# Kernel optimization log

Hardware: AMD Instinct MI355X
Metric: run time of the kernel (lower is better)

Reference implementation:

```python
import jax, jax.numpy as jnp
import numpy as np

N_NODES = 100000
N_EDGES = 400000
N_GRAPHS = 2500
DIM = 128
F_IN = 78
N_LAYERS = 3
BN_EPS = 1e-5


def setup_inputs() -> dict:
    key = jax.random.key(0)
    ks = jax.random.split(key, 24)
    def lin(k, fi, fo):
        return jax.random.normal(k, (fi, fo), jnp.float32) / np.sqrt(fi)
    inp = {
        "x": jax.random.normal(ks[0], (N_NODES, F_IN), jnp.float32),
        "edge_index": jax.random.randint(ks[1], (2, N_EDGES), 0, N_NODES, jnp.int32),
        "batch": jnp.sort(jax.random.randint(ks[2], (N_NODES,), 0, N_GRAPHS, jnp.int32)),
        "num_graphs": N_GRAPHS,
        "gcn1_W": lin(ks[3], F_IN, DIM), "gcn1_b": jnp.zeros((DIM,), jnp.float32),
        "gcn2_W": lin(ks[4], DIM, DIM), "gcn2_b": jnp.zeros((DIM,), jnp.float32),
        "gin0_w1": lin(ks[5], F_IN, DIM), "gin0_b1": jnp.zeros((DIM,), jnp.float32),
        "gin0_w2": lin(ks[6], DIM, DIM), "gin0_b2": jnp.zeros((DIM,), jnp.float32),
        # layers 1..2 stacked (same 128->128 shapes)
        "gin_w1": jnp.stack([lin(ks[7], DIM, DIM), lin(ks[8], DIM, DIM)]),
        "gin_b1": jnp.zeros((2, DIM), jnp.float32),
        "gin_w2": jnp.stack([lin(ks[9], DIM, DIM), lin(ks[10], DIM, DIM)]),
        "gin_b2": jnp.zeros((2, DIM), jnp.float32),
        "bn_gamma": jnp.ones((N_LAYERS, DIM), jnp.float32),
        "bn_beta": jnp.zeros((N_LAYERS, DIM), jnp.float32),
    }
    return inp


def reference(x, edge_index, batch, num_graphs,
              gcn1_W, gcn1_b, gcn2_W, gcn2_b,
              gin0_w1, gin0_b1, gin0_w2, gin0_b2,
              gin_w1, gin_b1, gin_w2, gin_b2,
              bn_gamma, bn_beta):
    n = x.shape[0]
    src, dst = edge_index[0], edge_index[1]

    def gcn(h, W, b):
        # linear -> symmetric-normalized aggregation with self loops (PyG GCNConv)
        h = h @ W
        loop = jnp.arange(n, dtype=src.dtype)
        s = jnp.concatenate([src, loop])
        d = jnp.concatenate([dst, loop])
        deg = jax.ops.segment_sum(jnp.ones(s.shape[0], h.dtype), d, num_segments=n)
        dis = jax.lax.rsqrt(deg)  # deg >= 1 thanks to self loops
        norm = (dis[s] * dis[d])[:, None]
        return jax.ops.segment_sum(h[s] * norm, d, num_segments=n) + b

    def gin(h, w1, b1, w2, b2):
        # GINConv, eps=0: mlp(x + sum_{j->i} x_j)
        agg = jax.ops.segment_sum(h[src], dst, num_segments=n)
        z = jax.nn.relu((h + agg) @ w1 + b1)
        return z @ w2 + b2

    def bn(h, g, bt):
        mu = h.mean(0)
        var = ((h - mu) ** 2).mean(0)
        return (h - mu) * jax.lax.rsqrt(var + BN_EPS) * g + bt

    g1 = jax.nn.relu(gcn(x, gcn1_W, gcn1_b))
    g2 = jax.nn.relu(gcn(g1, gcn2_W, gcn2_b))
    g2a = g2 + g1
    g2m = g2 * g1

    h = x
    xs = []
    m = jnp.float32(1.0)
    e = jnp.float32(0.0)
    for i in range(N_LAYERS):
        if i == 0:
            h = gin(h, gin0_w1, gin0_b1, gin0_w2, gin0_b2)
        else:
            h = gin(h, gin_w1[i - 1], gin_b1[i - 1], gin_w2[i - 1], gin_b2[i - 1])
        h = bn(jax.nn.relu(h), bn_gamma[i], bn_beta[i])
        m = m * h
        e = e + h
        xs.append(h)

    rep = jnp.concatenate(xs + [m, e, g1, g2, g2a, g2m], axis=-1)  # [N, 9*DIM]
    return jax.ops.segment_max(rep, batch, num_segments=num_graphs)
```

## Files before the change

### kernel.cpp

```cpp
#include <hip/hip_runtime.h>
#include <math.h>

#define DIMC 128
#define FINC 78
#define REPW 1152
#define SCAN_TILE 1024

typedef __attribute__((ext_vector_type(8))) short short8x;
typedef __attribute__((ext_vector_type(4))) float f32x4;
typedef unsigned int u32;
typedef const __attribute__((address_space(1))) u32* gas_u32p;
typedef __attribute__((address_space(3))) u32* las_u32p;

__device__ inline float b2f(unsigned short u) {
    union { unsigned int i; float f; } v; v.i = ((unsigned int)u) << 16; return v.f;
}
__device__ inline unsigned short f2b(float f) {
    union { float f; unsigned int i; } v; v.f = f;
    unsigned int r = (v.i + 0x7FFFu + ((v.i >> 16) & 1u)) >> 16;
    return (unsigned short)r;
}

__device__ __forceinline__ void gld16(const void* g, void* l) {
    __builtin_amdgcn_global_load_lds((gas_u32p)g, (las_u32p)l, 16, 0, 0);
}


__global__ void k_fill_int(int* __restrict__ p, int v, int n) {
    int i = blockIdx.x * blockDim.x + threadIdx.x;
    if (i < n) p[i] = v;
}

__global__ void k_fill(float* __restrict__ p, float v, int n) {
    int i = blockIdx.x * blockDim.x + threadIdx.x;
    if (i < n) p[i] = v;
}

__global__ void k_count(const int* __restrict__ dst, int* __restrict__ cnt, int E) {
    int e = blockIdx.x * blockDim.x + threadIdx.x;
    if (e < E) atomicAdd(&cnt[dst[e]], 1);
}

__launch_bounds__(256)
__global__ void k_tilesum(const int* __restrict__ cnt, int* __restrict__ tileSum, int N) {
    __shared__ int red[256];
    int base = blockIdx.x * SCAN_TILE;
    int s = 0;
    for (int i = threadIdx.x; i < SCAN_TILE; i += 256) {
        int idx = base + i;
        if (idx < N) s += cnt[idx];
    }
    red[threadIdx.x] = s;
    __syncthreads();
    for (int d = 128; d > 0; d >>= 1) {
        if (threadIdx.x < d) red[threadIdx.x] += red[threadIdx.x + d];
        __syncthreads();
    }
    if (threadIdx.x == 0) tileSum[blockIdx.x] = red[0];
}

__launch_bounds__(256)
__global__ void k_tilescan(const int* __restrict__ tileSum, int* __restrict__ tileOff,
                           int* __restrict__ rowptr, int T, int N) {
    __shared__ int sh[256];
    int t = threadIdx.x;
    int orig = (t < T) ? tileSum[t] : 0;
    sh[t] = orig;
    __syncthreads();
    for (int d = 1; d < 256; d <<= 1) {
        int v = (t >= d) ? sh[t - d] : 0;
        __syncthreads();
        sh[t] += v;
        __syncthreads();
    }
    if (t < T) tileOff[t] = sh[t] - orig;
    if (t == 255) rowptr[N] = sh[255];
}

__launch_bounds__(256)
__global__ void k_tileemit(const int* __restrict__ cnt, const int* __restrict__ tileOff,
                           int* __restrict__ rowptr, int* __restrict__ cursor,
                           float* __restrict__ dis, int N) {
    __shared__ int sh[256];
    int t = threadIdx.x;
    int base = blockIdx.x * SCAN_TILE;
    int idx0 = base + t * 4;
    int v0 = 0, v1 = 0, v2 = 0, v3 = 0;
    if (idx0 + 3 < N) {
        int4 v = *(const int4*)(cnt + idx0);
        v0 = v.x; v1 = v.y; v2 = v.z; v3 = v.w;
    } else {
        if (idx0 + 0 < N) v0 = cnt[idx0 + 0];
        if (idx0 + 1 < N) v1 = cnt[idx0 + 1];
        if (idx0 + 2 < N) v2 = cnt[idx0 + 2];
        if (idx0 + 3 < N) v3 = cnt[idx0 + 3];
    }
    int s0 = v0, s1 = s0 + v1, s2 = s1 + v2, s3 = s2 + v3;
    sh[t] = s3;
    __syncthreads();
    for (int d = 1; d < 256; d <<= 1) {
        int v = (t >= d) ? sh[t - d] : 0;
        __syncthreads();
        sh[t] += v;
        __syncthreads();
    }
    int gbase = tileOff[blockIdx.x] + ((t == 0) ? 0 : sh[t - 1]);
    int ex[4] = {0, s0, s1, s2};
    int vv[4] = {v0, v1, v2, v3};
#pragma unroll
    for (int j = 0; j < 4; ++j) {
        int idx = idx0 + j;
        if (idx < N) {
            int r = gbase + ex[j];
            rowptr[idx] = r;
            cursor[idx] = r;
            dis[idx] = rsqrtf((float)vv[j] + 1.0f);
        }
    }
}

__global__ void k_scatter(const int* __restrict__ src, const int* __restrict__ dst,
                          int* __restrict__ cursor, int* __restrict__ col, int E) {
    int e = blockIdx.x * blockDim.x + threadIdx.x;
    if (e < E) {
        int pos = atomicAdd(&cursor[dst[e]], 1);
        col[pos] = src[e];
    }
}

__global__ void k_bounds(const int* __restrict__ batch, int* __restrict__ start, int N, int G) {
    int g = blockIdx.x * blockDim.x + threadIdx.x;
    if (g <= G) {
        int lo = 0, hi = N;
        while (lo < hi) { int mid = (lo + hi) >> 1; if (batch[mid] < g) lo = mid + 1; else hi = mid; }
        start[g] = lo;
    }
}


__global__ void k_cvt_w(const float* __restrict__ s0, const float* __restrict__ s1,
                        const float* __restrict__ s2, const float* __restrict__ s3,
                        const float* __restrict__ s4, const float* __restrict__ s5,
                        const float* __restrict__ s6, const float* __restrict__ s7,
                        unsigned short* __restrict__ whi, unsigned short* __restrict__ wlo) {
    int my = blockIdx.y;
    const float* src; int Ksrc, KP; size_t dstoff;
    const size_t o96 = (size_t)128 * 96, o128 = (size_t)128 * 128;
    switch (my) {
        case 0: src = s0; Ksrc = 78;  KP = 96;  dstoff = 0; break;
        case 1: src = s1; Ksrc = 78;  KP = 96;  dstoff = o96; break;
        case 2: src = s2; Ksrc = 128; KP = 128; dstoff = 2 * o96; break;
        case 3: src = s3; Ksrc = 128; KP = 128; dstoff = 2 * o96 + o128; break;
        case 4: src = s4; Ksrc = 128; KP = 128; dstoff = 2 * o96 + 2 * o128; break;
        case 5: src = s5; Ksrc = 128; KP = 128; dstoff = 2 * o96 + 3 * o128; break;
        case 6: src = s6; Ksrc = 128; KP = 128; dstoff = 2 * o96 + 4 * o128; break;
        default: src = s7; Ksrc = 128; KP = 128; dstoff = 2 * o96 + 5 * o128; break;
    }
    int i = blockIdx.x * blockDim.x + threadIdx.x;
    if (i < 128 * KP) {
        int n = i / KP, k = i - n * KP;
        float v = (k < Ksrc) ? src[(size_t)k * DIMC + n] : 0.f;
        unsigned short hi = f2b(v);
        unsigned short lo = f2b(v - b2f(hi));
        whi[dstoff + i] = hi;
        wlo[dstoff + i] = lo;
    }
}


__global__ void k_pack_x(const float* __restrict__ x, unsigned short* __restrict__ xhi,
                         unsigned short* __restrict__ xlo, int N) {
    int i = blockIdx.x * blockDim.x + threadIdx.x;
    int r = i / 24, cc = (i - r * 24) * 4;
    if (r >= N) return;
    float v[4];
#pragma unroll
    for (int j = 0; j < 4; ++j) { int k = cc + j; v[j] = (k < FINC) ? x[(size_t)r * FINC + k] : 0.f; }
    unsigned short h[4], l[4];
#pragma unroll
    for (int j = 0; j < 4; ++j) { h[j] = f2b(v[j]); l[j] = f2b(v[j] - b2f(h[j])); }
    *(ushort4*)(xhi + (size_t)r * 96 + cc) = make_ushort4(h[0], h[1], h[2], h[3]);
    *(ushort4*)(xlo + (size_t)r * 96 + cc) = make_ushort4(l[0], l[1], l[2], l[3]);
}


template<int KP, bool SPLITA, bool STATS>
__launch_bounds__(256, 3)
__global__ void k_gemm_f(const void* __restrict__ A0, const void* __restrict__ A1,
                         const unsigned short* __restrict__ Bhi, const unsigned short* __restrict__ Blo,
                         const float* __restrict__ bias, const float* __restrict__ rowScale,
                         float* __restrict__ statsOut, float* __restrict__ C,
                         int N, int doRelu) {
    constexpr int NT = KP / 32;
    __shared__ unsigned short lds[2][2][4096];
    __shared__ float sStats[256];
    const int tid = threadIdx.x;
    const int wave = tid >> 6, lane = tid & 63;
    const int lm = lane & 15, q = lane >> 4;
    const int row = blockIdx.x * 64 + wave * 16 + lm;
    const int am = (row < N) ? row : (N - 1);

    const int rr = tid & 127;
    const int g0 = tid >> 7;
    const int o0 = ((g0 ^ (rr & 3)) << 3);
    const int o1 = (((2 + g0) ^ (rr & 3)) << 3);
    const size_t brow = (size_t)rr * KP;
    const int u0 = tid << 3;
    const int u1 = (256 + tid) << 3;

    auto stageB = [&](int c, int d) {
        const int cb = c << 5;
        gld16(Bhi + brow + cb + o0, &lds[d][0][u0]);
        gld16(Bhi + brow + cb + o1, &lds[d][0][u1]);
        gld16(Blo + brow + cb + o0, &lds[d][1][u0]);
        gld16(Blo + brow + cb + o1, &lds[d][1][u1]);
    };

    const unsigned short* aph = nullptr;
    const unsigned short* apl = nullptr;
    const float* apf = nullptr;
    if constexpr (SPLITA) {
        aph = (const unsigned short*)A0 + (size_t)am * KP;
        apl = (const unsigned short*)A1 + (size_t)am * KP;
    } else {
        apf = (const float*)A0 + (size_t)am * KP;
    }

    short8x pah, pal, nah, nal;
    float4 pf0, pf1, nf0, nf1;

    auto loadA = [&](int c, short8x& h, short8x& l, float4& f0, float4& f1) {
        int ko = c * 32 + q * 8;
        if constexpr (SPLITA) {
            h = *(const short8x*)(aph + ko);
            l = *(const short8x*)(apl + ko);
        } else {
            f0 = *(const float4*)(apf + ko);
            f1 = *(const float4*)(apf + ko + 4);
        }
    };

    f32x4 acc[8];
#pragma unroll
    for (int i = 0; i < 8; ++i) acc[i] = (f32x4){0.f, 0.f, 0.f, 0.f};

    stageB(0, 0);
    loadA(0, pah, pal, pf0, pf1);
    __builtin_amdgcn_sched_barrier(0);

#pragma unroll
    for (int t = 0; t < NT; ++t) {
        const int cur = t & 1;
        if (t + 1 < NT) {
            stageB(t + 1, cur ^ 1);
            loadA(t + 1, nah, nal, nf0, nf1);
            __builtin_amdgcn_sched_barrier(0);
            asm volatile("s_waitcnt vmcnt(6)" ::: "memory");
        } else {
            asm volatile("s_waitcnt vmcnt(0)" ::: "memory");
        }
        __builtin_amdgcn_s_barrier();
        __builtin_amdgcn_sched_barrier(0);

        short8x ah, al;
        if constexpr (SPLITA) {
            ah = pah; al = pal;
        } else {
            float f[8] = {pf0.x, pf0.y, pf0.z, pf0.w, pf1.x, pf1.y, pf1.z, pf1.w};
#pragma unroll
            for (int j = 0; j < 8; ++j) {
                unsigned short h = f2b(f[j]);
                ah[j] = (short)h;
                al[j] = (short)f2b(f[j] - b2f(h));
            }
        }
#pragma unroll
        for (int ct = 0; ct < 8; ++ct) {
            int n = ct * 16 + lm;
            int sl = ((q ^ (n & 3)) * 128 + n) << 3;
            short8x bh = *(const short8x*)&lds[cur][0][sl];
            short8x bl = *(const short8x*)&lds[cur][1][sl];
            acc[ct] = __builtin_amdgcn_mfma_f32_16x16x32_bf16(bh, ah, acc[ct], 0, 0, 0);
            acc[ct] = __builtin_amdgcn_mfma_f32_16x16x32_bf16(bh, al, acc[ct], 0, 0, 0);
            acc[ct] = __builtin_amdgcn_mfma_f32_16x16x32_bf16(bl, ah, acc[ct], 0, 0, 0);
        }
        __builtin_amdgcn_s_barrier();
        pah = nah; pal = nal; pf0 = nf0; pf1 = nf1;
    }

    if constexpr (STATS) { sStats[tid] = 0.f; __syncthreads(); }
    const bool valid = row < N;
    float sc = 1.f;
    if (rowScale) sc = rowScale[valid ? row : 0];

#pragma unroll
    for (int ct = 0; ct < 8; ++ct) {
        float vv[4];
#pragma unroll
        for (int i = 0; i < 4; ++i) {
            float v = acc[ct][i];
            if (bias) v += bias[ct * 16 + q * 4 + i];
            if (doRelu) v = fmaxf(v, 0.f);
            v *= sc;
            vv[i] = valid ? v : 0.f;
        }
        if (valid)
            *(float4*)(C + (size_t)row * DIMC + ct * 16 + q * 4) =
                make_float4(vv[0], vv[1], vv[2], vv[3]);
        if constexpr (STATS) {
#pragma unroll
            for (int i = 0; i < 4; ++i) {
                float vs = vv[i], vq = vv[i] * vv[i];
#pragma unroll
                for (int o = 1; o < 16; o <<= 1) { vs += __shfl_xor(vs, o); vq += __shfl_xor(vq, o); }
                if (lm == 0) {
                    int colg = ct * 16 + q * 4 + i;
                    atomicAdd(&sStats[colg], vs);
                    atomicAdd(&sStats[DIMC + colg], vq);
                }
            }
        }
    }
    if constexpr (STATS) {
        __syncthreads();
        atomicAdd(&statsOut[tid], sStats[tid]);
    }
}


__global__ void k_bn_coef(const float* __restrict__ bnsum, const float* __restrict__ gamma,
                          const float* __restrict__ beta, float* __restrict__ coef, float invN) {
    int c = threadIdx.x;
    float mu  = bnsum[c] * invN;
    float var = bnsum[128 + c] * invN - mu * mu;
    float inv = rsqrtf(var + 1e-5f);
    float s = gamma[c] * inv;
    coef[c] = s;
    coef[128 + c] = beta[c] - mu * s;
}


__global__ void k_fold_w(const float* __restrict__ w1, const float* __restrict__ coefL,
                         unsigned short* __restrict__ fwhi, unsigned short* __restrict__ fwlo,
                         float* __restrict__ cvec) {
    __shared__ float red[128];
    int n = blockIdx.x, k = threadIdx.x;
    float w = w1[(size_t)k * DIMC + n];
    float ws = w * coefL[k];
    unsigned short h = f2b(ws);
    fwhi[(size_t)n * DIMC + k] = h;
    fwlo[(size_t)n * DIMC + k] = f2b(ws - b2f(h));
    red[k] = w * coefL[DIMC + k];
    __syncthreads();
    for (int d = 64; d > 0; d >>= 1) { if (k < d) red[k] += red[k + d]; __syncthreads(); }
    if (k == 0) cvec[n] = red[0];
}


__global__ void k_gather_gcn(const float4* __restrict__ t, const int* __restrict__ rowptr,
                             const int* __restrict__ col, const float* __restrict__ dis,
                             const float4* __restrict__ bias, float4* __restrict__ out, int N) {
    int i = blockIdx.x * blockDim.x + threadIdx.x;
    int node = i >> 5, c4 = i & 31;
    if (node >= N) return;
    int s = rowptr[node], e = rowptr[node + 1];
    float4 acc = t[(size_t)node * 32 + c4];
    for (int k = s; k < e; ++k) {
        float4 v = t[(size_t)col[k] * 32 + c4];
        acc.x += v.x; acc.y += v.y; acc.z += v.z; acc.w += v.w;
    }
    float d = dis[node];
    float4 b = bias[c4];
    float4 o;
    o.x = fmaxf(acc.x * d + b.x, 0.f);
    o.y = fmaxf(acc.y * d + b.y, 0.f);
    o.z = fmaxf(acc.z * d + b.z, 0.f);
    o.w = fmaxf(acc.w * d + b.w, 0.f);
    out[(size_t)node * 32 + c4] = o;
}

__global__ void k_gather_gin(const float4* __restrict__ t, const int* __restrict__ rowptr,
                             const int* __restrict__ col, const float4* __restrict__ bias,
                             float4* __restrict__ out, int N) {
    int i = blockIdx.x * blockDim.x + threadIdx.x;
    int node = i >> 5, c4 = i & 31;
    if (node >= N) return;
    int s = rowptr[node], e = rowptr[node + 1];
    float4 acc = t[(size_t)node * 32 + c4];
    for (int k = s; k < e; ++k) {
        float4 v = t[(size_t)col[k] * 32 + c4];
        acc.x += v.x; acc.y += v.y; acc.z += v.z; acc.w += v.w;
    }
    float4 b = bias[c4];
    float4 o;
    o.x = fmaxf(acc.x + b.x, 0.f);
    o.y = fmaxf(acc.y + b.y, 0.f);
    o.z = fmaxf(acc.z + b.z, 0.f);
    o.w = fmaxf(acc.w + b.w, 0.f);
    out[(size_t)node * 32 + c4] = o;
}


__global__ void k_segmax_gin_all(const float* __restrict__ h0, const float* __restrict__ h1,
                                 const float* __restrict__ h2, const float* __restrict__ coef,
                                 const int* __restrict__ start, float* __restrict__ out) {
    int g = blockIdx.x, c = threadIdx.x;
    float s0 = coef[c],       t0 = coef[128 + c];
    float s1 = coef[256 + c], t1 = coef[384 + c];
    float s2 = coef[512 + c], t2 = coef[640 + c];
    int s = start[g], e = start[g + 1];
    float m0 = -INFINITY, m1 = -INFINITY, m2 = -INFINITY, mm = -INFINITY, me = -INFINITY;
    for (int n = s; n < e; ++n) {
        size_t idx = (size_t)n * DIMC + c;
        float a0 = fmaf(h0[idx], s0, t0);
        float a1 = fmaf(h1[idx], s1, t1);
        float a2 = fmaf(h2[idx], s2, t2);
        m0 = fmaxf(m0, a0); m1 = fmaxf(m1, a1); m2 = fmaxf(m2, a2);
        mm = fmaxf(mm, a0 * a1 * a2);
        me = fmaxf(me, a0 + a1 + a2);
    }
    size_t o = (size_t)g * REPW + c;
    out[o]            = m0;
    out[o + 1 * DIMC] = m1;
    out[o + 2 * DIMC] = m2;
    out[o + 3 * DIMC] = mm;
    out[o + 4 * DIMC] = me;
}

__global__ void k_segmax_gcn(const float* __restrict__ G1, const float* __restrict__ G2,
                             const int* __restrict__ start, float* __restrict__ out) {
    int g = blockIdx.x, c = threadIdx.x;
    int s = start[g], e = start[g + 1];
    float m1 = -INFINITY, m2 = -INFINITY, ma = -INFINITY, mm = -INFINITY;
    for (int n = s; n < e; ++n) {
        float a = G1[(size_t)n * DIMC + c], b = G2[(size_t)n * DIMC + c];
        m1 = fmaxf(m1, a); m2 = fmaxf(m2, b);
        ma = fmaxf(ma, a + b); mm = fmaxf(mm, a * b);
    }
    size_t o = (size_t)g * REPW + c;
    out[o + 5 * DIMC] = m1;
    out[o + 6 * DIMC] = m2;
    out[o + 7 * DIMC] = ma;
    out[o + 8 * DIMC] = mm;
}


extern "C" void kernel_launch(void* const* d_in, const int* in_sizes, int n_in,
                              void* d_out, int out_size, void* d_ws, size_t ws_size,
                              hipStream_t stream) {
    const float* x       = (const float*)d_in[0];
    const int*   ei      = (const int*)d_in[1];
    const int*   batch   = (const int*)d_in[2];
    const float* gcn1_W  = (const float*)d_in[4];
    const float* gcn1_b  = (const float*)d_in[5];
    const float* gcn2_W  = (const float*)d_in[6];
    const float* gcn2_b  = (const float*)d_in[7];
    const float* gin0_w1 = (const float*)d_in[8];
    const float* gin0_b1 = (const float*)d_in[9];
    const float* gin0_w2 = (const float*)d_in[10];
    const float* gin0_b2 = (const float*)d_in[11];
    const float* gin_w1  = (const float*)d_in[12];
    const float* gin_b1  = (const float*)d_in[13];
    const float* gin_w2  = (const float*)d_in[14];
    const float* gin_b2  = (const float*)d_in[15];
    const float* bn_g    = (const float*)d_in[16];
    const float* bn_b    = (const float*)d_in[17];
    float* out = (float*)d_out;

    const int N = in_sizes[0] / FINC;
    const int E = in_sizes[1] / 2;
    const int G = out_size / REPW;
    const int* srcv = ei;
    const int* dstv = ei + E;

    char* ws = (char*)d_ws;
    size_t off = 0;
    auto alloc = [&](size_t bytes) { char* p = ws + off; off += (bytes + 255) & ~(size_t)255; return p; };
    int*   cnt     = (int*)alloc((size_t)N * 4);
    int*   rowptr  = (int*)alloc(((size_t)N + 1) * 4);
    int*   cursor  = (int*)alloc((size_t)N * 4);
    int*   col     = (int*)alloc((size_t)E * 4);
    float* dis     = (float*)alloc((size_t)N * 4);
    float* bnsum   = (float*)alloc(768 * 4);
    float* coef    = (float*)alloc(768 * 4);
    float* cvec    = (float*)alloc(128 * 4);
    int*   start   = (int*)alloc(((size_t)G + 1) * 4);
    int*   tileSum = (int*)alloc(256 * 4);
    int*   tileOff = (int*)alloc(256 * 4);
    const size_t o96 = (size_t)128 * 96, o128 = (size_t)128 * 128;
    const size_t wtElems = 2 * o96 + 6 * o128;
    unsigned short* whi  = (unsigned short*)alloc(wtElems * 2);
    unsigned short* wlo  = (unsigned short*)alloc(wtElems * 2);
    unsigned short* fwhi = (unsigned short*)alloc(o128 * 2);
    unsigned short* fwlo = (unsigned short*)alloc(o128 * 2);
    const size_t fbytes = (size_t)N * DIMC * 4;
    float* bufT = (float*)alloc(fbytes);
    float* bufZ = (float*)alloc(fbytes);
    float* h0   = (float*)alloc(fbytes);
    float* h1   = (float*)alloc(fbytes);
    float* h2   = (float*)alloc(fbytes);
    unsigned short* xhi = (unsigned short*)h1;
    unsigned short* xlo = (unsigned short*)h1 + (size_t)N * 96;
    (void)ws_size; (void)n_in;

    const size_t woff[8] = {0, o96, 2 * o96, 2 * o96 + o128, 2 * o96 + 2 * o128,
                            2 * o96 + 3 * o128, 2 * o96 + 4 * o128, 2 * o96 + 5 * o128};

    const int T = 256;
    auto cdiv = [](long a, long b) { return (int)((a + b - 1) / b); };
    const int gemmGrid = cdiv(N, 64);
    const int gatherGrid = cdiv((long)N * 32, T);
    const int nTiles = cdiv(N, SCAN_TILE);
    const float invN = 1.0f / (float)N;

    k_fill_int<<<cdiv(N, T), T, 0, stream>>>(cnt, 0, N);
    k_count<<<cdiv(E, T), T, 0, stream>>>(dstv, cnt, E);
    k_tilesum<<<nTiles, T, 0, stream>>>(cnt, tileSum, N);
    k_tilescan<<<1, T, 0, stream>>>(tileSum, tileOff, rowptr, nTiles, N);
    k_tileemit<<<nTiles, T, 0, stream>>>(cnt, tileOff, rowptr, cursor, dis, N);
    k_scatter<<<cdiv(E, T), T, 0, stream>>>(srcv, dstv, cursor, col, E);
    k_bounds<<<cdiv(G + 1, T), T, 0, stream>>>(batch, start, N, G);
    k_fill<<<3, T, 0, stream>>>(bnsum, 0.f, 768);
    {
        dim3 g(64, 8);
        k_cvt_w<<<g, T, 0, stream>>>(gcn1_W, gin0_w1, gcn2_W, gin0_w2,
                                     gin_w1, gin_w1 + o128, gin_w2, gin_w2 + o128, whi, wlo);
    }
    k_pack_x<<<cdiv((long)N * 24, T), T, 0, stream>>>(x, xhi, xlo, N);

    k_gemm_f<96, true, false><<<gemmGrid, T, 0, stream>>>(xhi, xlo, whi + woff[0], wlo + woff[0],
                                                          nullptr, dis, nullptr, bufT, N, 0);
    k_gather_gcn<<<gatherGrid, T, 0, stream>>>((const float4*)bufT, rowptr, col, dis,
                                               (const float4*)gcn1_b, (float4*)bufZ, N);
    k_gemm_f<128, false, false><<<gemmGrid, T, 0, stream>>>(bufZ, nullptr, whi + woff[2], wlo + woff[2],
                                                            nullptr, dis, nullptr, bufT, N, 0);
    k_gather_gcn<<<gatherGrid, T, 0, stream>>>((const float4*)bufT, rowptr, col, dis,
                                               (const float4*)gcn2_b, (float4*)h0, N);
    k_segmax_gcn<<<G, DIMC, 0, stream>>>(bufZ, h0, start, out);

    k_gemm_f<96, true, false><<<gemmGrid, T, 0, stream>>>(xhi, xlo, whi + woff[1], wlo + woff[1],
                                                          nullptr, nullptr, nullptr, bufT, N, 0);
    k_gather_gin<<<gatherGrid, T, 0, stream>>>((const float4*)bufT, rowptr, col,
                                               (const float4*)gin0_b1, (float4*)bufZ, N);
    k_gemm_f<128, false, true><<<gemmGrid, T, 0, stream>>>(bufZ, nullptr, whi + woff[3], wlo + woff[3],
                                                           gin0_b2, nullptr, bnsum, h0, N, 1);
    k_bn_coef<<<1, DIMC, 0, stream>>>(bnsum, bn_g, bn_b, coef, invN);
    k_fold_w<<<DIMC, DIMC, 0, stream>>>(gin_w1, coef, fwhi, fwlo, cvec);

    k_gemm_f<128, false, false><<<gemmGrid, T, 0, stream>>>(h0, nullptr, fwhi, fwlo,
                                                            cvec, nullptr, nullptr, bufT, N, 0);
    k_gather_gin<<<gatherGrid, T, 0, stream>>>((const float4*)bufT, rowptr, col,
                                               (const float4*)gin_b1, (float4*)bufZ, N);
    k_gemm_f<128, false, true><<<gemmGrid, T, 0, stream>>>(bufZ, nullptr, whi + woff[6], wlo + woff[6],
                                                           gin_b2, nullptr, bnsum + 256, h1, N, 1);
    k_bn_coef<<<1, DIMC, 0, stream>>>(bnsum + 256, bn_g + DIMC, bn_b + DIMC, coef + 256, invN);
    k_fold_w<<<DIMC, DIMC, 0, stream>>>(gin_w1 + o128, coef + 256, fwhi, fwlo, cvec);

    k_gemm_f<128, false, false><<<gemmGrid, T, 0, stream>>>(h1, nullptr, fwhi, fwlo,
                                                            cvec, nullptr, nullptr, bufT, N, 0);
    k_gather_gin<<<gatherGrid, T, 0, stream>>>((const float4*)bufT, rowptr, col,
                                               (const float4*)(gin_b1 + DIMC), (float4*)bufZ, N);
    k_gemm_f<128, false, true><<<gemmGrid, T, 0, stream>>>(bufZ, nullptr, whi + woff[7], wlo + woff[7],
                                                           gin_b2 + DIMC, nullptr, bnsum + 512, h2, N, 1);
    k_bn_coef<<<1, DIMC, 0, stream>>>(bnsum + 512, bn_g + 2 * DIMC, bn_b + 2 * DIMC, coef + 512, invN);

    k_segmax_gin_all<<<G, DIMC, 0, stream>>>(h0, h1, h2, coef, start, out);
}
```

Before: 818.0 us.

## Make GEMM persistent with full B resident in LDS and 32-row wave strips

Turns the split-bf16 GEMM into a persistent kernel with a fixed grid of 768 or 512 blocks. Each block loads the whole 128-wide weight matrix (hi and lo) into LDS once, then its waves loop over independent 32-row strips with no block barriers inside the loop. BN statistics now accumulate in registers across strips and are reduced only once per block, which cuts shared and global atomics. The cost is more LDS and registers per block (two accumulator sets, launch bounds lowered to 2), plus possible load imbalance from the fixed grid.

After: 1.125 ms. +37.5%, slower.

```diff
diff --git a/kernel.cpp b/kernel.cpp
--- a/kernel.cpp
+++ b/kernel.cpp
@@ -184,133 +184,174 @@
 }
 
 
+#define LOADA(c, H0, L0, H1, L1, F00, F01, F10, F11)                           \
+    {                                                                          \
+        const int ko_ = (c) * 32 + q * 8;                                      \
+        if constexpr (SPLITA) {                                                \
+            H0 = *(const short8x*)(aph0 + ko_);                                \
+            L0 = *(const short8x*)(apl0 + ko_);                                \
+            H1 = *(const short8x*)(aph1 + ko_);                                \
+            L1 = *(const short8x*)(apl1 + ko_);                                \
+        } else {                                                               \
+            F00 = *(const float4*)(apf0 + ko_);                                \
+            F01 = *(const float4*)(apf0 + ko_ + 4);                            \
+            F10 = *(const float4*)(apf1 + ko_);                                \
+            F11 = *(const float4*)(apf1 + ko_ + 4);                            \
+        }                                                                      \
+    }
+
+#define CVT8(F0, F1, H, L)                                                     \
+    {                                                                          \
+        float ff_[8] = {F0.x, F0.y, F0.z, F0.w, F1.x, F1.y, F1.z, F1.w};       \
+        _Pragma("unroll")                                                      \
+        for (int j_ = 0; j_ < 8; ++j_) {                                       \
+            unsigned short hh_ = f2b(ff_[j_]);                                 \
+            H[j_] = (short)hh_;                                                \
+            L[j_] = (short)f2b(ff_[j_] - b2f(hh_));                            \
+        }                                                                      \
+    }
+
+#define EPI(ROW, ACC)                                                          \
+    {                                                                          \
+        const int row_ = (ROW);                                                \
+        const bool valid_ = row_ < N;                                          \
+        float sc_ = 1.f;                                                       \
+        if (rowScale) sc_ = rowScale[valid_ ? row_ : 0];                       \
+        _Pragma("unroll")                                                      \
+        for (int ct_ = 0; ct_ < 8; ++ct_) {                                    \
+            float vv_[4];                                                      \
+            _Pragma("unroll")                                                  \
+            for (int i_ = 0; i_ < 4; ++i_) {                                   \
+                float v_ = ACC[ct_][i_];                                       \
+                if (bias) v_ += bias[ct_ * 16 + q * 4 + i_];                   \
+                if (doRelu) v_ = fmaxf(v_, 0.f);                               \
+                v_ *= sc_;                                                     \
+                vv_[i_] = valid_ ? v_ : 0.f;                                   \
+                if constexpr (STATS) {                                         \
+                    cs[ct_][i_] += vv_[i_];                                    \
+                    cq[ct_][i_] = fmaf(vv_[i_], vv_[i_], cq[ct_][i_]);         \
+                }                                                              \
+            }                                                                  \
+            if (valid_)                                                        \
+                *(float4*)(C + (size_t)row_ * DIMC + ct_ * 16 + q * 4) =       \
+                    make_float4(vv_[0], vv_[1], vv_[2], vv_[3]);               \
+        }                                                                      \
+    }
+
 template<int KP, bool SPLITA, bool STATS>
-__launch_bounds__(256, 3)
-__global__ void k_gemm_f(const void* __restrict__ A0, const void* __restrict__ A1,
+__launch_bounds__(256, 2)
+__global__ void k_gemm_s(const void* __restrict__ A0, const void* __restrict__ A1,
                          const unsigned short* __restrict__ Bhi, const unsigned short* __restrict__ Blo,
                          const float* __restrict__ bias, const float* __restrict__ rowScale,
                          float* __restrict__ statsOut, float* __restrict__ C,
-                         int N, int doRelu) {
+                         int N, int doRelu, int nStrips) {
     constexpr int NT = KP / 32;
-    __shared__ unsigned short lds[2][2][4096];
+    __shared__ unsigned short lds[NT][2][4096];
     __shared__ float sStats[256];
     const int tid = threadIdx.x;
     const int wave = tid >> 6, lane = tid & 63;
     const int lm = lane & 15, q = lane >> 4;
-    const int row = blockIdx.x * 64 + wave * 16 + lm;
-    const int am = (row < N) ? row : (N - 1);
-
-    const int rr = tid & 127;
-    const int g0 = tid >> 7;
-    const int o0 = ((g0 ^ (rr & 3)) << 3);
-    const int o1 = (((2 + g0) ^ (rr & 3)) << 3);
-    const size_t brow = (size_t)rr * KP;
-    const int u0 = tid << 3;
-    const int u1 = (256 + tid) << 3;
-
-    auto stageB = [&](int c, int d) {
-        const int cb = c << 5;
-        gld16(Bhi + brow + cb + o0, &lds[d][0][u0]);
-        gld16(Bhi + brow + cb + o1, &lds[d][0][u1]);
-        gld16(Blo + brow + cb + o0, &lds[d][1][u0]);
-        gld16(Blo + brow + cb + o1, &lds[d][1][u1]);
-    };
-
-    const unsigned short* aph = nullptr;
-    const unsigned short* apl = nullptr;
-    const float* apf = nullptr;
-    if constexpr (SPLITA) {
-        aph = (const unsigned short*)A0 + (size_t)am * KP;
-        apl = (const unsigned short*)A1 + (size_t)am * KP;
-    } else {
-        apf = (const float*)A0 + (size_t)am * KP;
-    }
-
-    short8x pah, pal, nah, nal;
-    float4 pf0, pf1, nf0, nf1;
-
-    auto loadA = [&](int c, short8x& h, short8x& l, float4& f0, float4& f1) {
-        int ko = c * 32 + q * 8;
+
+    if constexpr (STATS) sStats[tid] = 0.f;
+
+    {
+        const int rr = tid & 127;
+        const int g0 = tid >> 7;
+        const int o0 = ((g0 ^ (rr & 3)) << 3);
+        const int o1 = (((2 + g0) ^ (rr & 3)) << 3);
+        const size_t brow = (size_t)rr * KP;
+        const int u0 = tid << 3;
+        const int u1 = (256 + tid) << 3;
+#pragma unroll
+        for (int c = 0; c < NT; ++c) {
+            const int cb = c << 5;
+            gld16(Bhi + brow + cb + o0, &lds[c][0][u0]);
+            gld16(Bhi + brow + cb + o1, &lds[c][0][u1]);
+            gld16(Blo + brow + cb + o0, &lds[c][1][u0]);
+            gld16(Blo + brow + cb + o1, &lds[c][1][u1]);
+        }
+    }
+    asm volatile("s_waitcnt vmcnt(0)" ::: "memory");
+    __syncthreads();
+
+    float cs[8][4], cq[8][4];
+    if constexpr (STATS) {
+#pragma unroll
+        for (int a = 0; a < 8; ++a)
+#pragma unroll
+            for (int b = 0; b < 4; ++b) { cs[a][b] = 0.f; cq[a][b] = 0.f; }
+    }
+
+    const int gw = blockIdx.x * 4 + wave;
+    const int nw = gridDim.x * 4;
+
+    for (int s = gw; s < nStrips; s += nw) {
+        const int r0 = s * 32 + lm, r1 = r0 + 16;
+        const int a0 = (r0 < N) ? r0 : N - 1;
+        const int a1 = (r1 < N) ? r1 : N - 1;
+        const unsigned short *aph0 = nullptr, *apl0 = nullptr, *aph1 = nullptr, *apl1 = nullptr;
+        const float *apf0 = nullptr, *apf1 = nullptr;
         if constexpr (SPLITA) {
-            h = *(const short8x*)(aph + ko);
-            l = *(const short8x*)(apl + ko);
+            aph0 = (const unsigned short*)A0 + (size_t)a0 * KP;
+            apl0 = (const unsigned short*)A1 + (size_t)a0 * KP;
+            aph1 = (const unsigned short*)A0 + (size_t)a1 * KP;
+            apl1 = (const unsigned short*)A1 + (size_t)a1 * KP;
         } else {
-            f0 = *(const float4*)(apf + ko);
-            f1 = *(const float4*)(apf + ko + 4);
+            apf0 = (const float*)A0 + (size_t)a0 * KP;
+            apf1 = (const float*)A0 + (size_t)a1 * KP;
         }
-    };
-
-    f32x4 acc[8];
-#pragma unroll
-    for (int i = 0; i < 8; ++i) acc[i] = (f32x4){0.f, 0.f, 0.f, 0.f};
-
-    stageB(0, 0);
-    loadA(0, pah, pal, pf0, pf1);
-    __builtin_amdgcn_sched_barrier(0);
-
-#pragma unroll
-    for (int t = 0; t < NT; ++t) {
-        const int cur = t & 1;
-        if (t + 1 < NT) {
-            stageB(t + 1, cur ^ 1);
-            loadA(t + 1, nah, nal, nf0, nf1);
-            __builtin_amdgcn_sched_barrier(0);
-            asm volatile("s_waitcnt vmcnt(6)" ::: "memory");
-        } else {
-            asm volatile("s_waitcnt vmcnt(0)" ::: "memory");
+
+        short8x xh0, xl0, xh1, xl1, yh0, yl0, yh1, yl1;
+        float4 xf00, xf01, xf10, xf11, yf00, yf01, yf10, yf11;
+        LOADA(0, xh0, xl0, xh1, xl1, xf00, xf01, xf10, xf11);
+
+        f32x4 acc0[8], acc1[8];
+#pragma unroll
+        for (int i = 0; i < 8; ++i) {
+            acc0[i] = (f32x4){0.f, 0.f, 0.f, 0.f};
+            acc1[i] = (f32x4){0.f, 0.f, 0.f, 0.f};
         }
-        __builtin_amdgcn_s_barrier();
-        __builtin_amdgcn_sched_barrier(0);
-
-        short8x ah, al;
-        if constexpr (SPLITA) {
-            ah = pah; al = pal;
-        } else {
-            float f[8] = {pf0.x, pf0.y, pf0.z, pf0.w, pf1.x, pf1.y, pf1.z, pf1.w};
-#pragma unroll
-            for (int j = 0; j < 8; ++j) {
-                unsigned short h = f2b(f[j]);
-                ah[j] = (short)h;
-                al[j] = (short)f2b(f[j] - b2f(h));
+
+#pragma unroll
+        for (int t = 0; t < NT; ++t) {
+            if (t + 1 < NT) LOADA(t + 1, yh0, yl0, yh1, yl1, yf00, yf01, yf10, yf11);
+            short8x ah0, al0, ah1, al1;
+            if constexpr (SPLITA) {
+                ah0 = xh0; al0 = xl0; ah1 = xh1; al1 = xl1;
+            } else {
+                CVT8(xf00, xf01, ah0, al0);
+                CVT8(xf10, xf11, ah1, al1);
+            }
+#pragma unroll
+            for (int ct = 0; ct < 8; ++ct) {
+                int n = ct * 16 + lm;
+                int sl = ((q ^ (n & 3)) * 128 + n) << 3;
+                short8x bh = *(const short8x*)&lds[t][0][sl];
+                short8x bl = *(const short8x*)&lds[t][1][sl];
+                acc0[ct] = __builtin_amdgcn_mfma_f32_16x16x32_bf16(bh, ah0, acc0[ct], 0, 0, 0);
+                acc0[ct] = __builtin_amdgcn_mfma_f32_16x16x32_bf16(bh, al0, acc0[ct], 0, 0, 0);
+                acc0[ct] = __builtin_amdgcn_mfma_f32_16x16x32_bf16(bl, ah0, acc0[ct], 0, 0, 0);
+                acc1[ct] = __builtin_amdgcn_mfma_f32_16x16x32_bf16(bh, ah1, acc1[ct], 0, 0, 0);
+                acc1[ct] = __builtin_amdgcn_mfma_f32_16x16x32_bf16(bh, al1, acc1[ct], 0, 0, 0);
+                acc1[ct] = __builtin_amdgcn_mfma_f32_16x16x32_bf16(bl, ah1, acc1[ct], 0, 0, 0);
+            }
+            if (t + 1 < NT) {
+                xh0 = yh0; xl0 = yl0; xh1 = yh1; xl1 = yl1;
+                xf00 = yf00; xf01 = yf01; xf10 = yf10; xf11 = yf11;
             }
         }
-#pragma unroll
-        for (int ct = 0; ct < 8; ++ct) {
-            int n = ct * 16 + lm;
-            int sl = ((q ^ (n & 3)) * 128 + n) << 3;
-            short8x bh = *(const short8x*)&lds[cur][0][sl];
-            short8x bl = *(const short8x*)&lds[cur][1][sl];
-            acc[ct] = __builtin_amdgcn_mfma_f32_16x16x32_bf16(bh, ah, acc[ct], 0, 0, 0);
-            acc[ct] = __builtin_amdgcn_mfma_f32_16x16x32_bf16(bh, al, acc[ct], 0, 0, 0);
-            acc[ct] = __builtin_amdgcn_mfma_f32_16x16x32_bf16(bl, ah, acc[ct], 0, 0, 0);
-        }
-        __builtin_amdgcn_s_barrier();
-        pah = nah; pal = nal; pf0 = nf0; pf1 = nf1;
-    }
-
-    if constexpr (STATS) { sStats[tid] = 0.f; __syncthreads(); }
-    const bool valid = row < N;
-    float sc = 1.f;
-    if (rowScale) sc = rowScale[valid ? row : 0];
-
-#pragma unroll
-    for (int ct = 0; ct < 8; ++ct) {
-        float vv[4];
-#pragma unroll
-        for (int i = 0; i < 4; ++i) {
-            float v = acc[ct][i];
-            if (bias) v += bias[ct * 16 + q * 4 + i];
-            if (doRelu) v = fmaxf(v, 0.f);
-            v *= sc;
-            vv[i] = valid ? v : 0.f;
-        }
-        if (valid)
-            *(float4*)(C + (size_t)row * DIMC + ct * 16 + q * 4) =
-                make_float4(vv[0], vv[1], vv[2], vv[3]);
-        if constexpr (STATS) {
+
+        EPI(r0, acc0);
+        EPI(r1, acc1);
+    }
+
+    if constexpr (STATS) {
+        __syncthreads();
+#pragma unroll
+        for (int ct = 0; ct < 8; ++ct)
 #pragma unroll
             for (int i = 0; i < 4; ++i) {
-                float vs = vv[i], vq = vv[i] * vv[i];
+                float vs = cs[ct][i], vq = cq[ct][i];
 #pragma unroll
                 for (int o = 1; o < 16; o <<= 1) { vs += __shfl_xor(vs, o); vq += __shfl_xor(vq, o); }
                 if (lm == 0) {
@@ -319,9 +360,6 @@
                     atomicAdd(&sStats[DIMC + colg], vq);
                 }
             }
-        }
-    }
-    if constexpr (STATS) {
         __syncthreads();
         atomicAdd(&statsOut[tid], sStats[tid]);
     }
@@ -508,7 +546,9 @@
 
     const int T = 256;
     auto cdiv = [](long a, long b) { return (int)((a + b - 1) / b); };
-    const int gemmGrid = cdiv(N, 64);
+    const int nStrips = cdiv(N, 32);
+    const int g96 = 768;
+    const int g128 = 512;
     const int gatherGrid = cdiv((long)N * 32, T);
     const int nTiles = cdiv(N, SCAN_TILE);
     const float invN = 1.0f / (float)N;
@@ -528,40 +568,40 @@
     }
     k_pack_x<<<cdiv((long)N * 24, T), T, 0, stream>>>(x, xhi, xlo, N);
 
-    k_gemm_f<96, true, false><<<gemmGrid, T, 0, stream>>>(xhi, xlo, whi + woff[0], wlo + woff[0],
-                                                          nullptr, dis, nullptr, bufT, N, 0);
+    k_gemm_s<96, true, false><<<g96, T, 0, stream>>>(xhi, xlo, whi + woff[0], wlo + woff[0],
+                                                     nullptr, dis, nullptr, bufT, N, 0, nStrips);
     k_gather_gcn<<<gatherGrid, T, 0, stream>>>((const float4*)bufT, rowptr, col, dis,
                                                (const float4*)gcn1_b, (float4*)bufZ, N);
-    k_gemm_f<128, false, false><<<gemmGrid, T, 0, stream>>>(bufZ, nullptr, whi + woff[2], wlo + woff[2],
-                                                            nullptr, dis, nullptr, bufT, N, 0);
+    k_gemm_s<128, false, false><<<g128, T, 0, stream>>>(bufZ, nullptr, whi + woff[2], wlo + woff[2],
+                                                        nullptr, dis, nullptr, bufT, N, 0, nStrips);
     k_gather_gcn<<<gatherGrid, T, 0, stream>>>((const float4*)bufT, rowptr, col, dis,
                                                (const float4*)gcn2_b, (float4*)h0, N);
     k_segmax_gcn<<<G, DIMC, 0, stream>>>(bufZ, h0, start, out);
 
-    k_gemm_f<96, true, false><<<gemmGrid, T, 0, stream>>>(xhi, xlo, whi + woff[1], wlo + woff[1],
-                                                          nullptr, nullptr, nullptr, bufT, N, 0);
+    k_gemm_s<96, true, false><<<g96, T, 0, stream>>>(xhi, xlo, whi + woff[1], wlo + woff[1],
+                                                     nullptr, nullptr, nullptr, bufT, N, 0, nStrips);
     k_gather_gin<<<gatherGrid, T, 0, stream>>>((const float4*)bufT, rowptr, col,
                                                (const float4*)gin0_b1, (float4*)bufZ, N);
-    k_gemm_f<128, false, true><<<gemmGrid, T, 0, stream>>>(bufZ, nullptr, whi + woff[3], wlo + woff[3],
-                                                           gin0_b2, nullptr, bnsum, h0, N, 1);
+    k_gemm_s<128, false, true><<<g128, T, 0, stream>>>(bufZ, nullptr, whi + woff[3], wlo + woff[3],
+                                                       gin0_b2, nullptr, bnsum, h0, N, 1, nStrips);
     k_bn_coef<<<1, DIMC, 0, stream>>>(bnsum, bn_g, bn_b, coef, invN);
     k_fold_w<<<DIMC, DIMC, 0, stream>>>(gin_w1, coef, fwhi, fwlo, cvec);
 
-    k_gemm_f<128, false, false><<<gemmGrid, T, 0, stream>>>(h0, nullptr, fwhi, fwlo,
-                                                            cvec, nullptr, nullptr, bufT, N, 0);
+    k_gemm_s<128, false, false><<<g128, T, 0, stream>>>(h0, nullptr, fwhi, fwlo,
+                                                        cvec, nullptr, nullptr, bufT, N, 0, nStrips);
     k_gather_gin<<<gatherGrid, T, 0, stream>>>((const float4*)bufT, rowptr, col,
                                                (const float4*)gin_b1, (float4*)bufZ, N);
-    k_gemm_f<128, false, true><<<gemmGrid, T, 0, stream>>>(bufZ, nullptr, whi + woff[6], wlo + woff[6],
-                                                           gin_b2, nullptr, bnsum + 256, h1, N, 1);
+    k_gemm_s<128, false, true><<<g128, T, 0, stream>>>(bufZ, nullptr, whi + woff[6], wlo + woff[6],
+                                                       gin_b2, nullptr, bnsum + 256, h1, N, 1, nStrips);
     k_bn_coef<<<1, DIMC, 0, stream>>>(bnsum + 256, bn_g + DIMC, bn_b + DIMC, coef + 256, invN);
     k_fold_w<<<DIMC, DIMC, 0, stream>>>(gin_w1 + o128, coef + 256, fwhi, fwlo, cvec);
 
-    k_gemm_f<128, false, false><<<gemmGrid, T, 0, stream>>>(h1, nullptr, fwhi, fwlo,
-                                                            cvec, nullptr, nullptr, bufT, N, 0);
+    k_gemm_s<128, false, false><<<g128, T, 0, stream>>>(h1, nullptr, fwhi, fwlo,
+                                                        cvec, nullptr, nullptr, bufT, N, 0, nStrips);
     k_gather_gin<<<gatherGrid, T, 0, stream>>>((const float4*)bufT, rowptr, col,
                                                (const float4*)(gin_b1 + DIMC), (float4*)bufZ, N);
-    k_gemm_f<128, false, true><<<gemmGrid, T, 0, stream>>>(bufZ, nullptr, whi + woff[7], wlo + woff[7],
-                                                           gin_b2 + DIMC, nullptr, bnsum + 512, h2, N, 1);
+    k_gemm_s<128, false, true><<<g128, T, 0, stream>>>(bufZ, nullptr, whi + woff[7], wlo + woff[7],
+                                                       gin_b2 + DIMC, nullptr, bnsum + 512, h2, N, 1, nStrips);
     k_bn_coef<<<1, DIMC, 0, stream>>>(bnsum + 512, bn_g + 2 * DIMC, bn_b + 2 * DIMC, coef + 512, invN);
 
     k_segmax_gin_all<<<G, DIMC, 0, stream>>>(h0, h1, h2, coef, start, out);
```

## Stage GEMM A tiles into LDS via DMA with 128-row blocks

Applied to the files above, without the earlier changes.

Replaces the GEMM kernel with one that loads the fp32 A tile into swizzled LDS through global_load_lds alongside B, and processes 128 rows per block with two 16-row tiles per wave. Each B fragment read from LDS now feeds two row tiles, and the per-lane direct A loads are gone. The input x is now only padded to fp32 instead of being pre-split into bf16 hi/lo halves, so the split happens in-kernel for every GEMM. BN statistics are accumulated per thread before the shuffle reduction. In exchange, LDS use and register pressure go up (launch bounds drop to 2 blocks per CU), and the last block stages A rows past N without a bounds guard.

After: 786.3 us. -3.9%, faster.

```diff
diff --git a/kernel.cpp b/kernel.cpp
--- a/kernel.cpp
+++ b/kernel.cpp
@@ -168,149 +168,147 @@
 }
 
 
-__global__ void k_pack_x(const float* __restrict__ x, unsigned short* __restrict__ xhi,
-                         unsigned short* __restrict__ xlo, int N) {
+__global__ void k_pad_x(const float* __restrict__ x, float* __restrict__ x96, int N) {
     int i = blockIdx.x * blockDim.x + threadIdx.x;
-    int r = i / 24, cc = (i - r * 24) * 4;
+    int r = i / 24, c4 = (i - r * 24) * 4;
     if (r >= N) return;
     float v[4];
 #pragma unroll
-    for (int j = 0; j < 4; ++j) { int k = cc + j; v[j] = (k < FINC) ? x[(size_t)r * FINC + k] : 0.f; }
-    unsigned short h[4], l[4];
-#pragma unroll
-    for (int j = 0; j < 4; ++j) { h[j] = f2b(v[j]); l[j] = f2b(v[j] - b2f(h[j])); }
-    *(ushort4*)(xhi + (size_t)r * 96 + cc) = make_ushort4(h[0], h[1], h[2], h[3]);
-    *(ushort4*)(xlo + (size_t)r * 96 + cc) = make_ushort4(l[0], l[1], l[2], l[3]);
-}
-
-
-template<int KP, bool SPLITA, bool STATS>
-__launch_bounds__(256, 3)
-__global__ void k_gemm_f(const void* __restrict__ A0, const void* __restrict__ A1,
-                         const unsigned short* __restrict__ Bhi, const unsigned short* __restrict__ Blo,
-                         const float* __restrict__ bias, const float* __restrict__ rowScale,
-                         float* __restrict__ statsOut, float* __restrict__ C,
-                         int N, int doRelu) {
+    for (int j = 0; j < 4; ++j) { int k = c4 + j; v[j] = (k < FINC) ? x[(size_t)r * FINC + k] : 0.f; }
+    *(float4*)(x96 + (size_t)r * 96 + c4) = make_float4(v[0], v[1], v[2], v[3]);
+}
+
+
+template<int KP, bool STATS>
+__launch_bounds__(256, 2)
+__global__ void k_gemm_dma(const float* __restrict__ A,
+                           const unsigned short* __restrict__ Bhi,
+                           const unsigned short* __restrict__ Blo,
+                           const float* __restrict__ bias, const float* __restrict__ rowScale,
+                           float* __restrict__ statsOut, float* __restrict__ C,
+                           int N, int doRelu) {
     constexpr int NT = KP / 32;
-    __shared__ unsigned short lds[2][2][4096];
+    __shared__ float ldsA[2][4096];
+    __shared__ unsigned short ldsB[2][2][4096];
     __shared__ float sStats[256];
     const int tid = threadIdx.x;
     const int wave = tid >> 6, lane = tid & 63;
     const int lm = lane & 15, q = lane >> 4;
-    const int row = blockIdx.x * 64 + wave * 16 + lm;
-    const int am = (row < N) ? row : (N - 1);
+    const int row0 = blockIdx.x * 128;
+    const int mrow = wave * 32;
 
     const int rr = tid & 127;
     const int g0 = tid >> 7;
-    const int o0 = ((g0 ^ (rr & 3)) << 3);
-    const int o1 = (((2 + g0) ^ (rr & 3)) << 3);
+    const int bo0 = ((g0 ^ (rr & 3)) << 3);
+    const int bo1 = (((2 + g0) ^ (rr & 3)) << 3);
     const size_t brow = (size_t)rr * KP;
-    const int u0 = tid << 3;
-    const int u1 = (256 + tid) << 3;
-
-    auto stageB = [&](int c, int d) {
+    const int bu0 = tid << 3;
+    const int bu1 = (256 + tid) << 3;
+    const size_t arow = (size_t)(row0 + rr) * KP;
+    int asrc[4];
+#pragma unroll
+    for (int o = 0; o < 4; ++o) asrc[o] = (((2 * o + g0) ^ (rr & 7)) << 2);
+
+    auto stage = [&](int c, int d) {
         const int cb = c << 5;
-        gld16(Bhi + brow + cb + o0, &lds[d][0][u0]);
-        gld16(Bhi + brow + cb + o1, &lds[d][0][u1]);
-        gld16(Blo + brow + cb + o0, &lds[d][1][u0]);
-        gld16(Blo + brow + cb + o1, &lds[d][1][u1]);
+#pragma unroll
+        for (int o = 0; o < 4; ++o)
+            gld16(A + arow + cb + asrc[o], &ldsA[d][(o * 256 + tid) << 2]);
+        gld16(Bhi + brow + cb + bo0, &ldsB[d][0][bu0]);
+        gld16(Bhi + brow + cb + bo1, &ldsB[d][0][bu1]);
+        gld16(Blo + brow + cb + bo0, &ldsB[d][1][bu0]);
+        gld16(Blo + brow + cb + bo1, &ldsB[d][1][bu1]);
     };
 
-    const unsigned short* aph = nullptr;
-    const unsigned short* apl = nullptr;
-    const float* apf = nullptr;
-    if constexpr (SPLITA) {
-        aph = (const unsigned short*)A0 + (size_t)am * KP;
-        apl = (const unsigned short*)A1 + (size_t)am * KP;
-    } else {
-        apf = (const float*)A0 + (size_t)am * KP;
-    }
-
-    short8x pah, pal, nah, nal;
-    float4 pf0, pf1, nf0, nf1;
-
-    auto loadA = [&](int c, short8x& h, short8x& l, float4& f0, float4& f1) {
-        int ko = c * 32 + q * 8;
-        if constexpr (SPLITA) {
-            h = *(const short8x*)(aph + ko);
-            l = *(const short8x*)(apl + ko);
-        } else {
-            f0 = *(const float4*)(apf + ko);
-            f1 = *(const float4*)(apf + ko + 4);
-        }
-    };
-
-    f32x4 acc[8];
-#pragma unroll
-    for (int i = 0; i < 8; ++i) acc[i] = (f32x4){0.f, 0.f, 0.f, 0.f};
-
-    stageB(0, 0);
-    loadA(0, pah, pal, pf0, pf1);
-    __builtin_amdgcn_sched_barrier(0);
-
+    f32x4 acc[2][8];
+#pragma unroll
+    for (int a = 0; a < 2; ++a)
+#pragma unroll
+        for (int b = 0; b < 8; ++b) acc[a][b] = (f32x4){0.f, 0.f, 0.f, 0.f};
+
+    stage(0, 0);
 #pragma unroll
     for (int t = 0; t < NT; ++t) {
         const int cur = t & 1;
         if (t + 1 < NT) {
-            stageB(t + 1, cur ^ 1);
-            loadA(t + 1, nah, nal, nf0, nf1);
-            __builtin_amdgcn_sched_barrier(0);
-            asm volatile("s_waitcnt vmcnt(6)" ::: "memory");
+            stage(t + 1, cur ^ 1);
+            asm volatile("s_waitcnt vmcnt(8)" ::: "memory");
         } else {
             asm volatile("s_waitcnt vmcnt(0)" ::: "memory");
         }
         __builtin_amdgcn_s_barrier();
         __builtin_amdgcn_sched_barrier(0);
 
-        short8x ah, al;
-        if constexpr (SPLITA) {
-            ah = pah; al = pal;
-        } else {
-            float f[8] = {pf0.x, pf0.y, pf0.z, pf0.w, pf1.x, pf1.y, pf1.z, pf1.w};
+        short8x ah[2], al[2];
+#pragma unroll
+        for (int rt = 0; rt < 2; ++rt) {
+            int m = mrow + rt * 16 + lm;
+            int s0 = (2 * q) ^ (m & 7), s1 = (2 * q + 1) ^ (m & 7);
+            float4 f0 = *(const float4*)&ldsA[cur][(s0 * 128 + m) << 2];
+            float4 f1 = *(const float4*)&ldsA[cur][(s1 * 128 + m) << 2];
+            float ff[8] = {f0.x, f0.y, f0.z, f0.w, f1.x, f1.y, f1.z, f1.w};
 #pragma unroll
             for (int j = 0; j < 8; ++j) {
-                unsigned short h = f2b(f[j]);
-                ah[j] = (short)h;
-                al[j] = (short)f2b(f[j] - b2f(h));
+                unsigned short h = f2b(ff[j]);
+                ah[rt][j] = (short)h;
+                al[rt][j] = (short)f2b(ff[j] - b2f(h));
             }
         }
 #pragma unroll
         for (int ct = 0; ct < 8; ++ct) {
             int n = ct * 16 + lm;
             int sl = ((q ^ (n & 3)) * 128 + n) << 3;
-            short8x bh = *(const short8x*)&lds[cur][0][sl];
-            short8x bl = *(const short8x*)&lds[cur][1][sl];
-            acc[ct] = __builtin_amdgcn_mfma_f32_16x16x32_bf16(bh, ah, acc[ct], 0, 0, 0);
-            acc[ct] = __builtin_amdgcn_mfma_f32_16x16x32_bf16(bh, al, acc[ct], 0, 0, 0);
-            acc[ct] = __builtin_amdgcn_mfma_f32_16x16x32_bf16(bl, ah, acc[ct], 0, 0, 0);
+            short8x bh = *(const short8x*)&ldsB[cur][0][sl];
+            short8x bl = *(const short8x*)&ldsB[cur][1][sl];
+#pragma unroll
+            for (int rt = 0; rt < 2; ++rt) {
+                acc[rt][ct] = __builtin_amdgcn_mfma_f32_16x16x32_bf16(bh, ah[rt], acc[rt][ct], 0, 0, 0);
+                acc[rt][ct] = __builtin_amdgcn_mfma_f32_16x16x32_bf16(bh, al[rt], acc[rt][ct], 0, 0, 0);
+                acc[rt][ct] = __builtin_amdgcn_mfma_f32_16x16x32_bf16(bl, ah[rt], acc[rt][ct], 0, 0, 0);
+            }
         }
         __builtin_amdgcn_s_barrier();
-        pah = nah; pal = nal; pf0 = nf0; pf1 = nf1;
-    }
-
-    if constexpr (STATS) { sStats[tid] = 0.f; __syncthreads(); }
-    const bool valid = row < N;
-    float sc = 1.f;
-    if (rowScale) sc = rowScale[valid ? row : 0];
-
-#pragma unroll
-    for (int ct = 0; ct < 8; ++ct) {
-        float vv[4];
-#pragma unroll
-        for (int i = 0; i < 4; ++i) {
-            float v = acc[ct][i];
-            if (bias) v += bias[ct * 16 + q * 4 + i];
-            if (doRelu) v = fmaxf(v, 0.f);
-            v *= sc;
-            vv[i] = valid ? v : 0.f;
+    }
+
+    float cs[8][4], cq[8][4];
+    if constexpr (STATS) {
+#pragma unroll
+        for (int a = 0; a < 8; ++a)
+#pragma unroll
+            for (int b = 0; b < 4; ++b) { cs[a][b] = 0.f; cq[a][b] = 0.f; }
+    }
+
+#pragma unroll
+    for (int rt = 0; rt < 2; ++rt) {
+        int grow = row0 + mrow + rt * 16 + lm;
+        if (grow < N) {
+            float sc = rowScale ? rowScale[grow] : 1.f;
+#pragma unroll
+            for (int ct = 0; ct < 8; ++ct) {
+                float vv[4];
+#pragma unroll
+                for (int i = 0; i < 4; ++i) {
+                    float v = acc[rt][ct][i];
+                    if (bias) v += bias[ct * 16 + q * 4 + i];
+                    if (doRelu) v = fmaxf(v, 0.f);
+                    v *= sc;
+                    vv[i] = v;
+                    if constexpr (STATS) { cs[ct][i] += v; cq[ct][i] = fmaf(v, v, cq[ct][i]); }
+                }
+                *(float4*)(C + (size_t)grow * DIMC + ct * 16 + q * 4) =
+                    make_float4(vv[0], vv[1], vv[2], vv[3]);
+            }
         }
-        if (valid)
-            *(float4*)(C + (size_t)row * DIMC + ct * 16 + q * 4) =
-                make_float4(vv[0], vv[1], vv[2], vv[3]);
-        if constexpr (STATS) {
+    }
+
+    if constexpr (STATS) {
+        sStats[tid] = 0.f;
+        __syncthreads();
+#pragma unroll
+        for (int ct = 0; ct < 8; ++ct)
 #pragma unroll
             for (int i = 0; i < 4; ++i) {
-                float vs = vv[i], vq = vv[i] * vv[i];
+                float vs = cs[ct][i], vq = cq[ct][i];
 #pragma unroll
                 for (int o = 1; o < 16; o <<= 1) { vs += __shfl_xor(vs, o); vq += __shfl_xor(vq, o); }
                 if (lm == 0) {
@@ -319,9 +317,6 @@
                     atomicAdd(&sStats[DIMC + colg], vq);
                 }
             }
-        }
-    }
-    if constexpr (STATS) {
         __syncthreads();
         atomicAdd(&statsOut[tid], sStats[tid]);
     }
@@ -499,8 +494,7 @@
     float* h0   = (float*)alloc(fbytes);
     float* h1   = (float*)alloc(fbytes);
     float* h2   = (float*)alloc(fbytes);
-    unsigned short* xhi = (unsigned short*)h1;
-    unsigned short* xlo = (unsigned short*)h1 + (size_t)N * 96;
+    float* x96  = h1;
     (void)ws_size; (void)n_in;
 
     const size_t woff[8] = {0, o96, 2 * o96, 2 * o96 + o128, 2 * o96 + 2 * o128,
@@ -508,7 +502,7 @@
 
     const int T = 256;
     auto cdiv = [](long a, long b) { return (int)((a + b - 1) / b); };
-    const int gemmGrid = cdiv(N, 64);
+    const int gemmGrid = cdiv(N, 128);
     const int gatherGrid = cdiv((long)N * 32, T);
     const int nTiles = cdiv(N, SCAN_TILE);
     const float invN = 1.0f / (float)N;
@@ -526,42 +520,42 @@
         k_cvt_w<<<g, T, 0, stream>>>(gcn1_W, gin0_w1, gcn2_W, gin0_w2,
                                      gin_w1, gin_w1 + o128, gin_w2, gin_w2 + o128, whi, wlo);
     }
-    k_pack_x<<<cdiv((long)N * 24, T), T, 0, stream>>>(x, xhi, xlo, N);
-
-    k_gemm_f<96, true, false><<<gemmGrid, T, 0, stream>>>(xhi, xlo, whi + woff[0], wlo + woff[0],
-                                                          nullptr, dis, nullptr, bufT, N, 0);
+    k_pad_x<<<cdiv((long)N * 24, T), T, 0, stream>>>(x, x96, N);
+
+    k_gemm_dma<96, false><<<gemmGrid, T, 0, stream>>>(x96, whi + woff[0], wlo + woff[0],
+                                                      nullptr, dis, nullptr, bufT, N, 0);
     k_gather_gcn<<<gatherGrid, T, 0, stream>>>((const float4*)bufT, rowptr, col, dis,
                                                (const float4*)gcn1_b, (float4*)bufZ, N);
-    k_gemm_f<128, false, false><<<gemmGrid, T, 0, stream>>>(bufZ, nullptr, whi + woff[2], wlo + woff[2],
-                                                            nullptr, dis, nullptr, bufT, N, 0);
+    k_gemm_dma<128, false><<<gemmGrid, T, 0, stream>>>(bufZ, whi + woff[2], wlo + woff[2],
+                                                       nullptr, dis, nullptr, bufT, N, 0);
     k_gather_gcn<<<gatherGrid, T, 0, stream>>>((const float4*)bufT, rowptr, col, dis,
                                                (const float4*)gcn2_b, (float4*)h0, N);
     k_segmax_gcn<<<G, DIMC, 0, stream>>>(bufZ, h0, start, out);
 
-    k_gemm_f<96, true, false><<<gemmGrid, T, 0, stream>>>(xhi, xlo, whi + woff[1], wlo + woff[1],
-                                                          nullptr, nullptr, nullptr, bufT, N, 0);
+    k_gemm_dma<96, false><<<gemmGrid, T, 0, stream>>>(x96, whi + woff[1], wlo + woff[1],
+                                                      nullptr, nullptr, nullptr, bufT, N, 0);
     k_gather_gin<<<gatherGrid, T, 0, stream>>>((const float4*)bufT, rowptr, col,
                                                (const float4*)gin0_b1, (float4*)bufZ, N);
-    k_gemm_f<128, false, true><<<gemmGrid, T, 0, stream>>>(bufZ, nullptr, whi + woff[3], wlo + woff[3],
-                                                           gin0_b2, nullptr, bnsum, h0, N, 1);
+    k_gemm_dma<128, true><<<gemmGrid, T, 0, stream>>>(bufZ, whi + woff[3], wlo + woff[3],
+                                                      gin0_b2, nullptr, bnsum, h0, N, 1);
     k_bn_coef<<<1, DIMC, 0, stream>>>(bnsum, bn_g, bn_b, coef, invN);
     k_fold_w<<<DIMC, DIMC, 0, stream>>>(gin_w1, coef, fwhi, fwlo, cvec);
 
-    k_gemm_f<128, false, false><<<gemmGrid, T, 0, stream>>>(h0, nullptr, fwhi, fwlo,
-                                                            cvec, nullptr, nullptr, bufT, N, 0);
+    k_gemm_dma<128, false><<<gemmGrid, T, 0, stream>>>(h0, fwhi, fwlo,
+                                                       cvec, nullptr, nullptr, bufT, N, 0);
     k_gather_gin<<<gatherGrid, T, 0, stream>>>((const float4*)bufT, rowptr, col,
                                                (const float4*)gin_b1, (float4*)bufZ, N);
-    k_gemm_f<128, false, true><<<gemmGrid, T, 0, stream>>>(bufZ, nullptr, whi + woff[6], wlo + woff[6],
-                                                           gin_b2, nullptr, bnsum + 256, h1, N, 1);
+    k_gemm_dma<128, true><<<gemmGrid, T, 0, stream>>>(bufZ, whi + woff[6], wlo + woff[6],
+                                                      gin_b2, nullptr, bnsum + 256, h1, N, 1);
     k_bn_coef<<<1, DIMC, 0, stream>>>(bnsum + 256, bn_g + DIMC, bn_b + DIMC, coef + 256, invN);
     k_fold_w<<<DIMC, DIMC, 0, stream>>>(gin_w1 + o128, coef + 256, fwhi, fwlo, cvec);
 
-    k_gemm_f<128, false, false><<<gemmGrid, T, 0, stream>>>(h1, nullptr, fwhi, fwlo,
-                                                            cvec, nullptr, nullptr, bufT, N, 0);
+    k_gemm_dma<128, false><<<gemmGrid, T, 0, stream>>>(h1, fwhi, fwlo,
+                                                       cvec, nullptr, nullptr, bufT, N, 0);
     k_gather_gin<<<gatherGrid, T, 0, stream>>>((const float4*)bufT, rowptr, col,
                                                (const float4*)(gin_b1 + DIMC), (float4*)bufZ, N);
-    k_gemm_f<128, false, true><<<gemmGrid, T, 0, stream>>>(bufZ, nullptr, whi + woff[7], wlo + woff[7],
-                                                           gin_b2 + DIMC, nullptr, bnsum + 512, h2, N, 1);
+    k_gemm_dma<128, true><<<gemmGrid, T, 0, stream>>>(bufZ, whi + woff[7], wlo + woff[7],
+                                                      gin_b2 + DIMC, nullptr, bnsum + 512, h2, N, 1);
     k_bn_coef<<<1, DIMC, 0, stream>>>(bnsum + 512, bn_g + 2 * DIMC, bn_b + 2 * DIMC, coef + 512, invN);
 
     k_segmax_gin_all<<<G, DIMC, 0, stream>>>(h0, h1, h2, coef, start, out);
```
